# Kernel tuning notes

Hardware: AMD Instinct MI355X
Metric: run time of the kernel (lower is better)

Reference implementation:

```python
import jax, jax.numpy as jnp
import numpy as np

NUM_HEADS = 12


def setup_inputs() -> dict:
    key = jax.random.key(0)
    k1, k2, k3 = jax.random.split(key, 3)
    B, S, D = 2, 2048, 768
    x = jax.random.normal(k1, (B, S, D), dtype=jnp.float32)
    # torch Linear init: normal(std=0.002) weights, zero bias; stored as [in, out]
    W_qkv = jax.random.normal(k2, (D, 3 * D), dtype=jnp.float32) * 0.002
    b_qkv = jnp.zeros((3 * D,), dtype=jnp.float32)
    W_vw = jax.random.normal(k3, (D, D), dtype=jnp.float32) * 0.002
    b_vw = jnp.zeros((D,), dtype=jnp.float32)
    mask = jnp.ones((B, S), dtype=jnp.int32)  # padding mask, all valid
    return {"x": x, "W_qkv": W_qkv, "b_qkv": b_qkv, "W_vw": W_vw, "b_vw": b_vw, "mask": mask}


def reference(x, W_qkv, b_qkv, W_vw, b_vw, mask):
    B, S, D = x.shape
    H = NUM_HEADS
    Dh = D // H
    qkv = (x @ W_qkv + b_qkv).reshape(B, S, 3, H, Dh)
    q, k, v = qkv[:, :, 0], qkv[:, :, 1], qkv[:, :, 2]
    # [B, H, S, S] attention scores (full matrix, as in original)
    w = jnp.einsum('bshd,bzhd->bhsz', q, k)
    w = w / jnp.sqrt(jnp.asarray(Dh, dtype=x.dtype))  # scale=True
    # log-mask trick: padding mask [B,1,1,S] * causal tril [1,1,S,S]
    causal = jnp.tril(jnp.ones((S, S), dtype=x.dtype))
    wholemask = mask.astype(x.dtype)[:, None, None, :] * causal[None, None]
    w = w + jnp.log(wholemask)
    w = jax.nn.softmax(w, axis=-1)
    vw = jnp.einsum('bhsz,bzhd->bshd', w, v).reshape(B, S, D)
    return vw @ W_vw + b_vw
```

## Files before the change

kernel.cpp:

```cpp
#include <hip/hip_runtime.h>
#include <hip/hip_bf16.h>
#include <cmath>
#include <cstddef>

#define B_    2
#define S_    2048
#define D_    768
#define H_    12
#define DH_   64
#define NQKV_ 2304

typedef __attribute__((ext_vector_type(8))) short  short8;
typedef __attribute__((ext_vector_type(4))) short  short4v;
typedef __attribute__((ext_vector_type(4))) float  floatx4;

__device__ __forceinline__ unsigned short f2bf(float f) {
    union { __hip_bfloat16 h; unsigned short u; } cv;
    cv.h = __float2bfloat16(f);
    return cv.u;
}

__device__ __forceinline__ void stage16(const unsigned short* g, unsigned short* ldsbase, int lane) {
#if __has_builtin(__builtin_amdgcn_global_load_lds)
    __builtin_amdgcn_global_load_lds(
        (const __attribute__((address_space(1))) unsigned int*)g,
        (__attribute__((address_space(3))) unsigned int*)ldsbase, 16, 0, 0);
#else
    *(short8*)(ldsbase + lane * 8) = *(const short8*)g;
#endif
}

__global__ void cvt_x_kernel(const float* __restrict__ x, unsigned short* __restrict__ xb)
{
    int i = (blockIdx.x * 256 + threadIdx.x) * 8;
    float4 a = *(const float4*)(x + i);
    float4 b = *(const float4*)(x + i + 4);
    short8 v;
    v[0] = (short)f2bf(a.x); v[1] = (short)f2bf(a.y);
    v[2] = (short)f2bf(a.z); v[3] = (short)f2bf(a.w);
    v[4] = (short)f2bf(b.x); v[5] = (short)f2bf(b.y);
    v[6] = (short)f2bf(b.z); v[7] = (short)f2bf(b.w);
    *(short8*)(xb + i) = v;
}

__global__ void cvt_w_kernel(const float* __restrict__ Wq, const float* __restrict__ Wv,
                             unsigned short* __restrict__ WqT, unsigned short* __restrict__ WvT)
{
    const int z = blockIdx.z;
    const int N = z ? D_ : NQKV_;
    if ((int)blockIdx.x * 32 >= N) return;
    const float* W = z ? Wv : Wq;
    unsigned short* WT = z ? WvT : WqT;

    __shared__ float t[32][33];
    const int tx = threadIdx.x, ty = threadIdx.y;
    const int n0 = blockIdx.x * 32, k0 = blockIdx.y * 32;
    #pragma unroll
    for (int i = 0; i < 4; ++i)
        t[ty + i * 8][tx] = W[(size_t)(k0 + ty + i * 8) * N + n0 + tx];
    __syncthreads();
    #pragma unroll
    for (int i = 0; i < 4; ++i)
        WT[(size_t)(n0 + ty + i * 8) * 768 + k0 + tx] = f2bf(t[tx][ty + i * 8]);
}

__global__ void vt_kernel(const unsigned short* __restrict__ V, unsigned short* __restrict__ VT)
{
    __shared__ unsigned short t[64][72];
    const int bh = blockIdx.x, s0 = blockIdx.y * 64;
    const unsigned short* src = V + ((size_t)bh * S_ + s0) * DH_;
    const int r = threadIdx.x >> 3, c = (threadIdx.x & 7) * 8;
    #pragma unroll
    for (int it = 0; it < 2; ++it)
        *(short8*)&t[r + it * 32][c] = *(const short8*)(src + (size_t)(r + it * 32) * DH_ + c);
    __syncthreads();
    #pragma unroll
    for (int it = 0; it < 2; ++it) {
        int d = r + it * 32;
        short8 v;
        #pragma unroll
        for (int i = 0; i < 8; ++i) v[i] = (short)t[c + i][d];
        *(short8*)(VT + ((size_t)bh * DH_ + d) * S_ + s0 + c) = v;
    }
}

__global__ __launch_bounds__(256, 2)
void mm_qkv_kernel(const unsigned short* __restrict__ A, const unsigned short* __restrict__ BT,
                   const float* __restrict__ bias,
                   unsigned short* __restrict__ Qo, unsigned short* __restrict__ Ko,
                   unsigned short* __restrict__ Vo)
{
    __shared__ unsigned short As[128][32];
    __shared__ unsigned short Bs[128][32];
    const int tid = threadIdx.x;
    const int wid = tid >> 6, lane = tid & 63;
    const int q = lane >> 4, ln = lane & 15;
    const int wm = (wid & 1) * 64, wn = (wid >> 1) * 64;
    const int m0 = blockIdx.y * 128, n0 = blockIdx.x * 128;
    const int lrow = wid * 16 + (lane >> 2);
    const int lcol = (lane & 3) * 8;
    const unsigned short* Ag = A  + (size_t)(m0 + lrow) * 768 + lcol;
    const unsigned short* Bg = BT + (size_t)(n0 + lrow) * 768 + lcol;

    floatx4 acc[4][4] = {};
    for (int k0 = 0; k0 < 768; k0 += 32) {
        __syncthreads();
        stage16(Ag + k0,            &As[wid * 16][0],      lane);
        stage16(Ag + k0 + 64 * 768, &As[64 + wid * 16][0], lane);
        stage16(Bg + k0,            &Bs[wid * 16][0],      lane);
        stage16(Bg + k0 + 64 * 768, &Bs[64 + wid * 16][0], lane);
        __syncthreads();
        short8 af[4], bf[4];
        #pragma unroll
        for (int mt = 0; mt < 4; ++mt) af[mt] = *(const short8*)&As[wm + mt * 16 + ln][q * 8];
        #pragma unroll
        for (int nt = 0; nt < 4; ++nt) bf[nt] = *(const short8*)&Bs[wn + nt * 16 + ln][q * 8];
        #pragma unroll
        for (int mt = 0; mt < 4; ++mt)
            #pragma unroll
            for (int nt = 0; nt < 4; ++nt)
                acc[mt][nt] = __builtin_amdgcn_mfma_f32_16x16x32_bf16(af[mt], bf[nt], acc[mt][nt], 0, 0, 0);
    }

    const int t = n0 / 768;
    unsigned short* __restrict__ dst = (t == 0) ? Qo : ((t == 1) ? Ko : Vo);
    const float qscale = (t == 0) ? 0.18033688011112042f : 1.0f;
    const int colb = n0 - t * 768 + wn;
    float bv[4];
    #pragma unroll
    for (int nt = 0; nt < 4; ++nt) bv[nt] = bias[n0 + wn + nt * 16 + ln];
    #pragma unroll
    for (int mt = 0; mt < 4; ++mt)
        #pragma unroll
        for (int r = 0; r < 4; ++r) {
            int row = m0 + wm + mt * 16 + q * 4 + r;
            int bb = row >> 11, s = row & 2047;
            #pragma unroll
            for (int nt = 0; nt < 4; ++nt) {
                int col = colb + nt * 16 + ln;
                int h = col >> 6, d = col & 63;
                dst[((size_t)(bb * H_ + h) * S_ + s) * DH_ + d] = f2bf((acc[mt][nt][r] + bv[nt]) * qscale);
            }
        }
}

__global__ __launch_bounds__(512, 2)
void flash13_kernel(const unsigned short* __restrict__ Qg, const unsigned short* __restrict__ Kg,
                    const unsigned short* __restrict__ VTg, const int* __restrict__ mask,
                    unsigned short* __restrict__ VW)
{
    __shared__ unsigned short Ks[3][32][64];
    __shared__ unsigned short Vs[3][64][32];
    __shared__ unsigned short Pl[8][16][40];

    const int tid = threadIdx.x;
    const int wid = tid >> 6, lane = tid & 63;
    const int q = lane >> 4, ln = lane & 15;
    const int bh = blockIdx.x % 24;
    const int j  = 15 - blockIdx.x / 24;
    const int b = bh / H_, h = bh % H_;
    const int r0w = j * 128 + wid * 16;
    const int T  = 4 * j + 4;
    const int Lw = 4 * j + (wid >> 1) + 1;

    const unsigned short* Qb = Qg  + (size_t)bh * S_ * DH_;
    const unsigned short* Kb = Kg  + (size_t)bh * S_ * DH_;
    const unsigned short* Vt = VTg + (size_t)bh * DH_ * S_;
    const int* mb = mask + b * S_;

    const bool isK = (wid < 4);
    const int krow = (wid & 3) * 8 + (lane >> 3);
    const int kslt = ((lane & 7) ^ (lane >> 3)) * 8;
    const int vrow = (wid & 3) * 16 + (lane >> 2);
    const int vslt = ((lane & 3) ^ ((lane >> 2) & 3)) * 8;

    short8 qf[2];
    #pragma unroll
    for (int kk = 0; kk < 2; ++kk)
        qf[kk] = *(const short8*)(Qb + (size_t)(r0w + ln) * DH_ + kk * 32 + q * 8);

    int am = 1;
    for (int zz = 0; zz < T * 32; zz += 512) {
        int v[8];
        #pragma unroll
        for (int u = 0; u < 8; ++u) {
            int z = zz + u * 64 + lane;
            v[u] = (z < T * 32) ? mb[z] : 1;
        }
        #pragma unroll
        for (int u = 0; u < 8; ++u) am &= (v[u] != 0);
    }
    const bool allmask = __all(am != 0);

    asm volatile("" ::: "memory");

    if (isK) {
        stage16(Kb + (size_t)(0 * 32 + krow) * DH_ + kslt, &Ks[0][(wid & 3) * 8][0], lane);
        stage16(Kb + (size_t)(1 * 32 + krow) * DH_ + kslt, &Ks[1][(wid & 3) * 8][0], lane);
    } else {
        stage16(Vt + (size_t)vrow * S_ + 0 * 32 + vslt, &Vs[0][(wid & 3) * 16][0], lane);
        stage16(Vt + (size_t)vrow * S_ + 1 * 32 + vslt, &Vs[1][(wid & 3) * 16][0], lane);
    }

    floatx4 o[4] = {};
    float li = 0.0f;

    for (int t = 0; t < T; ++t) {
        asm volatile("s_waitcnt vmcnt(1)" ::: "memory");
        __builtin_amdgcn_s_barrier();
        __builtin_amdgcn_sched_barrier(0);

        {
            const int ts = (t + 2 < T) ? (t + 2) : (T - 1);
            int wb = ts - (ts / 3) * 3;
            if (isK)
                stage16(Kb + (size_t)(ts * 32 + krow) * DH_ + kslt, &Ks[wb][(wid & 3) * 8][0], lane);
            else
                stage16(Vt + (size_t)vrow * S_ + ts * 32 + vslt, &Vs[wb][(wid & 3) * 16][0], lane);
        }

        if (t >= Lw) continue;
        const int cb = t - (t / 3) * 3;
        const int z0 = t * 32;

        short8 kf[2][2];
        #pragma unroll
        for (int zt = 0; zt < 2; ++zt)
            #pragma unroll
            for (int kk = 0; kk < 2; ++kk)
                kf[zt][kk] = *(const short8*)&Ks[cb][zt * 16 + ln][(((kk * 4 + q) ^ (ln & 7)) * 8)];

        short8 vb[4];
        #pragma unroll
        for (int dt = 0; dt < 4; ++dt)
            vb[dt] = *(const short8*)&Vs[cb][dt * 16 + ln][((q ^ (ln & 3)) * 8)];

        floatx4 s[2] = {};
        __builtin_amdgcn_s_setprio(1);
        #pragma unroll
        for (int zt = 0; zt < 2; ++zt) {
            s[zt] = __builtin_amdgcn_mfma_f32_16x16x32_bf16(kf[zt][0], qf[0], s[zt], 0, 0, 0);
            s[zt] = __builtin_amdgcn_mfma_f32_16x16x32_bf16(kf[zt][1], qf[1], s[zt], 0, 0, 0);
        }
        __builtin_amdgcn_s_setprio(0);

        const bool diag = (t == Lw - 1);
        if (allmask && !diag) {
            #pragma unroll
            for (int zt = 0; zt < 2; ++zt) {
                float p0 = exp2f(s[zt][0]);
                float p1 = exp2f(s[zt][1]);
                float p2 = exp2f(s[zt][2]);
                float p3 = exp2f(s[zt][3]);
                li += (p0 + p1) + (p2 + p3);
                short4v pk;
                pk[0] = (short)f2bf(p0); pk[1] = (short)f2bf(p1);
                pk[2] = (short)f2bf(p2); pk[3] = (short)f2bf(p3);
                *(short4v*)&Pl[wid][ln][zt * 16 + q * 4] = pk;
            }
        } else {
            const int4 mA = *(const int4*)&mb[z0 + q * 4];
            const int4 mB = *(const int4*)&mb[z0 + 16 + q * 4];
            int ma[2][4];
            ma[0][0] = mA.x; ma[0][1] = mA.y; ma[0][2] = mA.z; ma[0][3] = mA.w;
            ma[1][0] = mB.x; ma[1][1] = mB.y; ma[1][2] = mB.z; ma[1][3] = mB.w;
            #pragma unroll
            for (int zt = 0; zt < 2; ++zt) {
                const int zb = z0 + zt * 16 + q * 4;
                const int r  = r0w + ln;
                float p[4];
                #pragma unroll
                for (int rr = 0; rr < 4; ++rr) {
                    p[rr] = exp2f(s[zt][rr]);
                    if (!ma[zt][rr] || (zb + rr > r)) p[rr] = 0.0f;
                }
                li += (p[0] + p[1]) + (p[2] + p[3]);
                short4v pk;
                pk[0] = (short)f2bf(p[0]); pk[1] = (short)f2bf(p[1]);
                pk[2] = (short)f2bf(p[2]); pk[3] = (short)f2bf(p[3]);
                *(short4v*)&Pl[wid][ln][zt * 16 + q * 4] = pk;
            }
        }

        {
            short8 a = *(const short8*)&Pl[wid][ln][q * 8];
            __builtin_amdgcn_s_setprio(1);
            #pragma unroll
            for (int dt = 0; dt < 4; ++dt)
                o[dt] = __builtin_amdgcn_mfma_f32_16x16x32_bf16(a, vb[dt], o[dt], 0, 0, 0);
            __builtin_amdgcn_s_setprio(0);
        }
    }

    li += __shfl_xor(li, 16);
    li += __shfl_xor(li, 32);

    float inv[4];
    #pragma unroll
    for (int rr = 0; rr < 4; ++rr)
        inv[rr] = 1.0f / __shfl(li, q * 4 + rr);
    #pragma unroll
    for (int rr = 0; rr < 4; ++rr) {
        int srow = r0w + q * 4 + rr;
        unsigned short* dst = VW + ((size_t)b * S_ + srow) * D_ + h * DH_ + ln;
        #pragma unroll
        for (int dt = 0; dt < 4; ++dt)
            dst[dt * 16] = f2bf(o[dt][rr] * inv[rr]);
    }
}

__global__ __launch_bounds__(256, 2)
void mm_proj_kernel(const unsigned short* __restrict__ A, const unsigned short* __restrict__ BT,
                    const float* __restrict__ bias, float* __restrict__ C)
{
    __shared__ unsigned short As[128][32];
    __shared__ unsigned short Bs[64][32];
    const int tid = threadIdx.x;
    const int wid = tid >> 6, lane = tid & 63;
    const int q = lane >> 4, ln = lane & 15;
    const int wm = (wid & 1) * 64, wn = (wid >> 1) * 32;
    const int m0 = blockIdx.y * 128, n0 = blockIdx.x * 64;
    const int lrow = wid * 16 + (lane >> 2);
    const int lcol = (lane & 3) * 8;
    const unsigned short* Ag = A  + (size_t)(m0 + lrow) * 768 + lcol;
    const unsigned short* Bg = BT + (size_t)(n0 + lrow) * 768 + lcol;

    floatx4 acc[4][2] = {};
    for (int k0 = 0; k0 < 768; k0 += 32) {
        __syncthreads();
        stage16(Ag + k0,            &As[wid * 16][0],      lane);
        stage16(Ag + k0 + 64 * 768, &As[64 + wid * 16][0], lane);
        stage16(Bg + k0,            &Bs[wid * 16][0],      lane);
        __syncthreads();
        short8 af[4], bf[2];
        #pragma unroll
        for (int mt = 0; mt < 4; ++mt) af[mt] = *(const short8*)&As[wm + mt * 16 + ln][q * 8];
        #pragma unroll
        for (int nt = 0; nt < 2; ++nt) bf[nt] = *(const short8*)&Bs[wn + nt * 16 + ln][q * 8];
        #pragma unroll
        for (int mt = 0; mt < 4; ++mt)
            #pragma unroll
            for (int nt = 0; nt < 2; ++nt)
                acc[mt][nt] = __builtin_amdgcn_mfma_f32_16x16x32_bf16(af[mt], bf[nt], acc[mt][nt], 0, 0, 0);
    }

    float bv[2];
    #pragma unroll
    for (int nt = 0; nt < 2; ++nt) bv[nt] = bias[n0 + wn + nt * 16 + ln];
    #pragma unroll
    for (int mt = 0; mt < 4; ++mt)
        #pragma unroll
        for (int r = 0; r < 4; ++r) {
            size_t row = (size_t)m0 + wm + mt * 16 + q * 4 + r;
            #pragma unroll
            for (int nt = 0; nt < 2; ++nt)
                C[row * D_ + n0 + wn + nt * 16 + ln] = acc[mt][nt][r] + bv[nt];
        }
}

extern "C" void kernel_launch(void* const* d_in, const int* in_sizes, int n_in,
                              void* d_out, int out_size, void* d_ws, size_t ws_size,
                              hipStream_t stream)
{
    (void)in_sizes; (void)n_in; (void)out_size; (void)ws_size;
    const float* x    = (const float*)d_in[0];
    const float* Wqkv = (const float*)d_in[1];
    const float* bqkv = (const float*)d_in[2];
    const float* Wvw  = (const float*)d_in[3];
    const float* bvw  = (const float*)d_in[4];
    const int*   mask = (const int*)d_in[5];
    float* out = (float*)d_out;

    const size_t XN  = (size_t)B_ * S_ * D_;
    unsigned short* ws  = (unsigned short*)d_ws;
    unsigned short* xb  = ws;
    unsigned short* WqT = xb  + XN;
    unsigned short* WvT = WqT + (size_t)NQKV_ * D_;
    unsigned short* Qb  = WvT + (size_t)D_ * D_;
    unsigned short* Kb  = Qb + XN;
    unsigned short* Vb  = Kb + XN;
    unsigned short* VbT = Vb + XN;
    unsigned short* VW  = VbT + XN;

    cvt_x_kernel<<<dim3(XN / (256 * 8)), 256, 0, stream>>>(x, xb);
    cvt_w_kernel<<<dim3(NQKV_ / 32, D_ / 32, 2), dim3(32, 8), 0, stream>>>(Wqkv, Wvw, WqT, WvT);
    mm_qkv_kernel<<<dim3(NQKV_ / 128, (B_ * S_) / 128), 256, 0, stream>>>(xb, WqT, bqkv, Qb, Kb, Vb);
    vt_kernel<<<dim3(B_ * H_, S_ / 64), 256, 0, stream>>>(Vb, VbT);
    flash13_kernel<<<dim3(24 * 16), 512, 0, stream>>>(Qb, Kb, VbT, mask, VW);
    mm_proj_kernel<<<dim3(D_ / 64, (B_ * S_) / 128), 256, 0, stream>>>(VW, WvT, bvw, out);
}
```

Measured before the change: 182.5 us.

## Drop LDS K/V staging, load fragments directly and pair causal query tiles

Rewrites the attention kernel so each 256-thread block handles two 64-row query tiles (j and 31-j) to balance causal work. K and V^T fragments are now read straight from global memory into registers instead of going through a triple-buffered LDS pipeline with barriers, and the all-valid mask check is done per key tile with a wave vote. This removes block-wide barriers and LDS traffic and raises the occupancy target, but it gives up K/V sharing across waves and prefetch overlap, relying on the caches to absorb the repeated global loads.

After: 244.5 us. 34.0% more time.

```diff
diff --git a/kernel.cpp b/kernel.cpp
--- a/kernel.cpp
+++ b/kernel.cpp
@@ -144,168 +144,128 @@
         }
 }
 
-__global__ __launch_bounds__(512, 2)
-void flash13_kernel(const unsigned short* __restrict__ Qg, const unsigned short* __restrict__ Kg,
+__global__ __launch_bounds__(256, 4)
+void flash15_kernel(const unsigned short* __restrict__ Qg, const unsigned short* __restrict__ Kg,
                     const unsigned short* __restrict__ VTg, const int* __restrict__ mask,
                     unsigned short* __restrict__ VW)
 {
-    __shared__ unsigned short Ks[3][32][64];
-    __shared__ unsigned short Vs[3][64][32];
-    __shared__ unsigned short Pl[8][16][40];
+    __shared__ unsigned short Pl[4][16][40];
 
     const int tid = threadIdx.x;
     const int wid = tid >> 6, lane = tid & 63;
     const int q = lane >> 4, ln = lane & 15;
     const int bh = blockIdx.x % 24;
-    const int j  = 15 - blockIdx.x / 24;
+    const int p  = blockIdx.x / 24;
     const int b = bh / H_, h = bh % H_;
-    const int r0w = j * 128 + wid * 16;
-    const int T  = 4 * j + 4;
-    const int Lw = 4 * j + (wid >> 1) + 1;
 
     const unsigned short* Qb = Qg  + (size_t)bh * S_ * DH_;
     const unsigned short* Kb = Kg  + (size_t)bh * S_ * DH_;
     const unsigned short* Vt = VTg + (size_t)bh * DH_ * S_;
     const int* mb = mask + b * S_;
 
-    const bool isK = (wid < 4);
-    const int krow = (wid & 3) * 8 + (lane >> 3);
-    const int kslt = ((lane & 7) ^ (lane >> 3)) * 8;
-    const int vrow = (wid & 3) * 16 + (lane >> 2);
-    const int vslt = ((lane & 3) ^ ((lane >> 2) & 3)) * 8;
-
-    short8 qf[2];
-    #pragma unroll
-    for (int kk = 0; kk < 2; ++kk)
-        qf[kk] = *(const short8*)(Qb + (size_t)(r0w + ln) * DH_ + kk * 32 + q * 8);
-
-    int am = 1;
-    for (int zz = 0; zz < T * 32; zz += 512) {
-        int v[8];
-        #pragma unroll
-        for (int u = 0; u < 8; ++u) {
-            int z = zz + u * 64 + lane;
-            v[u] = (z < T * 32) ? mb[z] : 1;
-        }
-        #pragma unroll
-        for (int u = 0; u < 8; ++u) am &= (v[u] != 0);
-    }
-    const bool allmask = __all(am != 0);
-
-    asm volatile("" ::: "memory");
-
-    if (isK) {
-        stage16(Kb + (size_t)(0 * 32 + krow) * DH_ + kslt, &Ks[0][(wid & 3) * 8][0], lane);
-        stage16(Kb + (size_t)(1 * 32 + krow) * DH_ + kslt, &Ks[1][(wid & 3) * 8][0], lane);
-    } else {
-        stage16(Vt + (size_t)vrow * S_ + 0 * 32 + vslt, &Vs[0][(wid & 3) * 16][0], lane);
-        stage16(Vt + (size_t)vrow * S_ + 1 * 32 + vslt, &Vs[1][(wid & 3) * 16][0], lane);
-    }
-
-    floatx4 o[4] = {};
-    float li = 0.0f;
-
-    for (int t = 0; t < T; ++t) {
-        asm volatile("s_waitcnt vmcnt(1)" ::: "memory");
-        __builtin_amdgcn_s_barrier();
-        __builtin_amdgcn_sched_barrier(0);
-
-        {
-            const int ts = (t + 2 < T) ? (t + 2) : (T - 1);
-            int wb = ts - (ts / 3) * 3;
-            if (isK)
-                stage16(Kb + (size_t)(ts * 32 + krow) * DH_ + kslt, &Ks[wb][(wid & 3) * 8][0], lane);
-            else
-                stage16(Vt + (size_t)vrow * S_ + ts * 32 + vslt, &Vs[wb][(wid & 3) * 16][0], lane);
-        }
-
-        if (t >= Lw) continue;
-        const int cb = t - (t / 3) * 3;
-        const int z0 = t * 32;
-
-        short8 kf[2][2];
-        #pragma unroll
-        for (int zt = 0; zt < 2; ++zt)
-            #pragma unroll
-            for (int kk = 0; kk < 2; ++kk)
-                kf[zt][kk] = *(const short8*)&Ks[cb][zt * 16 + ln][(((kk * 4 + q) ^ (ln & 7)) * 8)];
-
-        short8 vb[4];
-        #pragma unroll
-        for (int dt = 0; dt < 4; ++dt)
-            vb[dt] = *(const short8*)&Vs[cb][dt * 16 + ln][((q ^ (ln & 3)) * 8)];
-
-        floatx4 s[2] = {};
-        __builtin_amdgcn_s_setprio(1);
-        #pragma unroll
-        for (int zt = 0; zt < 2; ++zt) {
-            s[zt] = __builtin_amdgcn_mfma_f32_16x16x32_bf16(kf[zt][0], qf[0], s[zt], 0, 0, 0);
-            s[zt] = __builtin_amdgcn_mfma_f32_16x16x32_bf16(kf[zt][1], qf[1], s[zt], 0, 0, 0);
-        }
-        __builtin_amdgcn_s_setprio(0);
-
-        const bool diag = (t == Lw - 1);
-        if (allmask && !diag) {
+    #pragma unroll
+    for (int ph = 0; ph < 2; ++ph) {
+        const int j = ph ? p : (31 - p);
+        const int r0w = j * 64 + wid * 16;
+        const int Tw = ((r0w + 15) >> 5) + 1;
+
+        short8 qf[2];
+        #pragma unroll
+        for (int kk = 0; kk < 2; ++kk)
+            qf[kk] = *(const short8*)(Qb + (size_t)(r0w + ln) * DH_ + kk * 32 + q * 8);
+
+        floatx4 o[4] = {};
+        float li = 0.0f;
+
+        for (int t = 0; t < Tw; ++t) {
+            const int z0 = t * 32;
+
+            short8 kf[2][2];
+            #pragma unroll
+            for (int zt = 0; zt < 2; ++zt)
+                #pragma unroll
+                for (int kk = 0; kk < 2; ++kk)
+                    kf[zt][kk] = *(const short8*)(Kb + (size_t)(z0 + zt * 16 + ln) * DH_ + kk * 32 + q * 8);
+
+            short8 vb[4];
+            #pragma unroll
+            for (int dt = 0; dt < 4; ++dt)
+                vb[dt] = *(const short8*)(Vt + (size_t)(dt * 16 + ln) * S_ + z0 + q * 8);
+
+            const int mi = mb[z0 + (lane & 31)];
+
+            floatx4 s[2] = {};
+            __builtin_amdgcn_s_setprio(1);
             #pragma unroll
             for (int zt = 0; zt < 2; ++zt) {
-                float p0 = exp2f(s[zt][0]);
-                float p1 = exp2f(s[zt][1]);
-                float p2 = exp2f(s[zt][2]);
-                float p3 = exp2f(s[zt][3]);
-                li += (p0 + p1) + (p2 + p3);
-                short4v pk;
-                pk[0] = (short)f2bf(p0); pk[1] = (short)f2bf(p1);
-                pk[2] = (short)f2bf(p2); pk[3] = (short)f2bf(p3);
-                *(short4v*)&Pl[wid][ln][zt * 16 + q * 4] = pk;
+                s[zt] = __builtin_amdgcn_mfma_f32_16x16x32_bf16(kf[zt][0], qf[0], s[zt], 0, 0, 0);
+                s[zt] = __builtin_amdgcn_mfma_f32_16x16x32_bf16(kf[zt][1], qf[1], s[zt], 0, 0, 0);
             }
-        } else {
-            const int4 mA = *(const int4*)&mb[z0 + q * 4];
-            const int4 mB = *(const int4*)&mb[z0 + 16 + q * 4];
-            int ma[2][4];
-            ma[0][0] = mA.x; ma[0][1] = mA.y; ma[0][2] = mA.z; ma[0][3] = mA.w;
-            ma[1][0] = mB.x; ma[1][1] = mB.y; ma[1][2] = mB.z; ma[1][3] = mB.w;
-            #pragma unroll
-            for (int zt = 0; zt < 2; ++zt) {
-                const int zb = z0 + zt * 16 + q * 4;
-                const int r  = r0w + ln;
-                float p[4];
+            __builtin_amdgcn_s_setprio(0);
+
+            const bool diag = (t == Tw - 1);
+            if (__all(mi != 0) && !diag) {
                 #pragma unroll
-                for (int rr = 0; rr < 4; ++rr) {
-                    p[rr] = exp2f(s[zt][rr]);
-                    if (!ma[zt][rr] || (zb + rr > r)) p[rr] = 0.0f;
+                for (int zt = 0; zt < 2; ++zt) {
+                    float p0 = exp2f(s[zt][0]);
+                    float p1 = exp2f(s[zt][1]);
+                    float p2 = exp2f(s[zt][2]);
+                    float p3 = exp2f(s[zt][3]);
+                    li += (p0 + p1) + (p2 + p3);
+                    short4v pk;
+                    pk[0] = (short)f2bf(p0); pk[1] = (short)f2bf(p1);
+                    pk[2] = (short)f2bf(p2); pk[3] = (short)f2bf(p3);
+                    *(short4v*)&Pl[wid][ln][zt * 16 + q * 4] = pk;
                 }
-                li += (p[0] + p[1]) + (p[2] + p[3]);
-                short4v pk;
-                pk[0] = (short)f2bf(p[0]); pk[1] = (short)f2bf(p[1]);
-                pk[2] = (short)f2bf(p[2]); pk[3] = (short)f2bf(p[3]);
-                *(short4v*)&Pl[wid][ln][zt * 16 + q * 4] = pk;
+            } else {
+                const int4 mA = *(const int4*)&mb[z0 + q * 4];
+                const int4 mB = *(const int4*)&mb[z0 + 16 + q * 4];
+                int ma[2][4];
+                ma[0][0] = mA.x; ma[0][1] = mA.y; ma[0][2] = mA.z; ma[0][3] = mA.w;
+                ma[1][0] = mB.x; ma[1][1] = mB.y; ma[1][2] = mB.z; ma[1][3] = mB.w;
+                #pragma unroll
+                for (int zt = 0; zt < 2; ++zt) {
+                    const int zb = z0 + zt * 16 + q * 4;
+                    const int r  = r0w + ln;
+                    float pv[4];
+                    #pragma unroll
+                    for (int rr = 0; rr < 4; ++rr) {
+                        pv[rr] = exp2f(s[zt][rr]);
+                        if (!ma[zt][rr] || (zb + rr > r)) pv[rr] = 0.0f;
+                    }
+                    li += (pv[0] + pv[1]) + (pv[2] + pv[3]);
+                    short4v pk;
+                    pk[0] = (short)f2bf(pv[0]); pk[1] = (short)f2bf(pv[1]);
+                    pk[2] = (short)f2bf(pv[2]); pk[3] = (short)f2bf(pv[3]);
+                    *(short4v*)&Pl[wid][ln][zt * 16 + q * 4] = pk;
+                }
+            }
+
+            {
+                short8 a = *(const short8*)&Pl[wid][ln][q * 8];
+                __builtin_amdgcn_s_setprio(1);
+                #pragma unroll
+                for (int dt = 0; dt < 4; ++dt)
+                    o[dt] = __builtin_amdgcn_mfma_f32_16x16x32_bf16(a, vb[dt], o[dt], 0, 0, 0);
+                __builtin_amdgcn_s_setprio(0);
             }
         }
 
-        {
-            short8 a = *(const short8*)&Pl[wid][ln][q * 8];
-            __builtin_amdgcn_s_setprio(1);
+        li += __shfl_xor(li, 16);
+        li += __shfl_xor(li, 32);
+
+        float inv[4];
+        #pragma unroll
+        for (int rr = 0; rr < 4; ++rr)
+            inv[rr] = 1.0f / __shfl(li, q * 4 + rr);
+        #pragma unroll
+        for (int rr = 0; rr < 4; ++rr) {
+            int srow = r0w + q * 4 + rr;
+            unsigned short* dst = VW + ((size_t)b * S_ + srow) * D_ + h * DH_ + ln;
             #pragma unroll
             for (int dt = 0; dt < 4; ++dt)
-                o[dt] = __builtin_amdgcn_mfma_f32_16x16x32_bf16(a, vb[dt], o[dt], 0, 0, 0);
-            __builtin_amdgcn_s_setprio(0);
+                dst[dt * 16] = f2bf(o[dt][rr] * inv[rr]);
         }
-    }
-
-    li += __shfl_xor(li, 16);
-    li += __shfl_xor(li, 32);
-
-    float inv[4];
-    #pragma unroll
-    for (int rr = 0; rr < 4; ++rr)
-        inv[rr] = 1.0f / __shfl(li, q * 4 + rr);
-    #pragma unroll
-    for (int rr = 0; rr < 4; ++rr) {
-        int srow = r0w + q * 4 + rr;
-        unsigned short* dst = VW + ((size_t)b * S_ + srow) * D_ + h * DH_ + ln;
-        #pragma unroll
-        for (int dt = 0; dt < 4; ++dt)
-            dst[dt * 16] = f2bf(o[dt][rr] * inv[rr]);
     }
 }
 
@@ -386,6 +346,6 @@
     cvt_w_kernel<<<dim3(NQKV_ / 32, D_ / 32, 2), dim3(32, 8), 0, stream>>>(Wqkv, Wvw, WqT, WvT);
     mm_qkv_kernel<<<dim3(NQKV_ / 128, (B_ * S_) / 128), 256, 0, stream>>>(xb, WqT, bqkv, Qb, Kb, Vb);
     vt_kernel<<<dim3(B_ * H_, S_ / 64), 256, 0, stream>>>(Vb, VbT);
-    flash13_kernel<<<dim3(24 * 16), 512, 0, stream>>>(Qb, Kb, VbT, mask, VW);
+    flash15_kernel<<<dim3(24 * 16), 256, 0, stream>>>(Qb, Kb, VbT, mask, VW);
     mm_proj_kernel<<<dim3(D_ / 64, (B_ * S_) / 128), 256, 0, stream>>>(VW, WvT, bvw, out);
 }
```
